# Performance work log

Measured on AMD Instinct MI355X. Metric: run time of the kernel, lower is better.

The kernel has to match this reference:

```python
import jax, jax.numpy as jnp
import numpy as np

B, S, E, H, STEPS = 32, 2048, 300, 256, 24


def setup_inputs() -> dict:
    key = jax.random.key(0)
    ks = jax.random.split(key, 16)
    sc = 0.05
    inp = {
        "input_ids": jax.random.normal(ks[0], (B, S, E), dtype=jnp.float32),
        "tree_ids": jax.random.randint(ks[1], (B, STEPS, S), 0, S),
        "tree_ids_r": jax.random.randint(ks[2], (B, STEPS, S), 0, S),
        "tree_ids_l": jax.random.randint(ks[3], (B, STEPS, S), 0, S),
        # N-ary (binary) TreeLSTM parameters (Tai et al. 2015)
        "W_iou": jax.random.normal(ks[4], (E, 3 * H), dtype=jnp.float32) * sc,
        "b_iou": jnp.zeros((3 * H,), dtype=jnp.float32),
        "U_iou_l": jax.random.normal(ks[5], (H, 3 * H), dtype=jnp.float32) * sc,
        "U_iou_r": jax.random.normal(ks[6], (H, 3 * H), dtype=jnp.float32) * sc,
        "W_f": jax.random.normal(ks[7], (E, H), dtype=jnp.float32) * sc,
        "b_f": jnp.zeros((H,), dtype=jnp.float32),
        "U_f_ll": jax.random.normal(ks[8], (H, H), dtype=jnp.float32) * sc,
        "U_f_lr": jax.random.normal(ks[9], (H, H), dtype=jnp.float32) * sc,
        "U_f_rl": jax.random.normal(ks[10], (H, H), dtype=jnp.float32) * sc,
        "U_f_rr": jax.random.normal(ks[11], (H, H), dtype=jnp.float32) * sc,
    }
    return inp


def _gather_nodes(t, idx):
    # t: [B,S,H], idx: [B,S] -> [B,S,H]
    return jnp.take_along_axis(t, idx[..., None], axis=1)


def reference(input_ids, tree_ids, tree_ids_r, tree_ids_l,
              W_iou, b_iou, U_iou_l, U_iou_r,
              W_f, b_f, U_f_ll, U_f_lr, U_f_rl, U_f_rr):
    dt = input_ids.dtype
    h0 = jnp.zeros((B, S, H), dtype=dt)
    c0 = jnp.zeros((B, S, H), dtype=dt)
    # input projections are step-invariant: compute once
    x_iou = input_ids @ W_iou + b_iou          # [B,S,3H]
    x_f = input_ids @ W_f + b_f                # [B,S,H]
    bidx = jnp.arange(B)[:, None]              # [B,1]

    def step(carry, ids):
        h, c = carry
        idd, idl, idr = ids                    # each [B,S]
        h_l = _gather_nodes(h, idl); c_l = _gather_nodes(c, idl)
        h_r = _gather_nodes(h, idr); c_r = _gather_nodes(c, idr)
        iou = x_iou + h_l @ U_iou_l + h_r @ U_iou_r
        i, o, u = jnp.split(iou, 3, axis=-1)
        i = jax.nn.sigmoid(i); o = jax.nn.sigmoid(o); u = jnp.tanh(u)
        f_l = jax.nn.sigmoid(x_f + h_l @ U_f_ll + h_r @ U_f_lr)
        f_r = jax.nn.sigmoid(x_f + h_l @ U_f_rl + h_r @ U_f_rr)
        c_new = i * u + f_l * c_l + f_r * c_r
        h_new = o * jnp.tanh(c_new)
        # scatter updates to destination node ids; slot 0 is the null slot
        h = h.at[bidx, idd].set(h_new)
        c = c.at[bidx, idd].set(c_new)
        h = h.at[:, 0].set(0.0)
        c = c.at[:, 0].set(0.0)
        return (h, c), None

    ids_seq = (jnp.transpose(tree_ids, (1, 0, 2)),
               jnp.transpose(tree_ids_l, (1, 0, 2)),
               jnp.transpose(tree_ids_r, (1, 0, 2)))
    (h, c), _ = jax.lax.scan(step, (h0, c0), ids_seq)

    roots = tree_ids[:, -1, :].max(axis=1)     # [B]
    h_root = jnp.take_along_axis(
        h, jnp.broadcast_to(roots[:, None, None], (B, 1, H)), axis=1)[:, 0]
    return (h, c, h_root)
```

## Files before the change

### kernel.cpp

```cpp
#include <hip/hip_runtime.h>
#include <hip/hip_bf16.h>
#include <math.h>

#define B_     32
#define S_     2048
#define E_     300
#define H_     256
#define STEPS_ 24
#define BS_    (B_ * S_)
#define NPACK  1280
#define KSL    16
#define KSLP   10
#define COPYB  1024

typedef __bf16 bf16x8 __attribute__((ext_vector_type(8)));
typedef float  f32x4  __attribute__((ext_vector_type(4)));

__device__ __forceinline__ float sigm(float x) {
    return 1.0f / (1.0f + __expf(-x));
}
__device__ __forceinline__ float fast_tanh(float x) {
    return 2.0f * sigm(2.0f * x) - 1.0f;
}

__global__ __launch_bounds__(256) void pack_B_kernel(
    const float* __restrict__ U_iou_l, const float* __restrict__ U_iou_r,
    const float* __restrict__ U_f_ll,  const float* __restrict__ U_f_lr,
    const float* __restrict__ U_f_rl,  const float* __restrict__ U_f_rr,
    __hip_bfloat16* __restrict__ Bp)
{
    const int idx = blockIdx.x * 256 + threadIdx.x;
    if (idx >= KSL * NPACK * 32) return;
    const int ks = idx / (NPACK * 32);
    const int rem = idx - ks * (NPACK * 32);
    const int p = rem >> 5;
    const int kin = rem & 31;
    const int k = ks * 32 + kin;
    const int w = p / 80;
    const int rg = p - w * 80;
    const int g = rg >> 4;
    const int c = w * 16 + (rg & 15);
    float v;
    if (g < 3) {
        const int col = g * 256 + c;
        v = (k < 256) ? U_iou_l[k * 768 + col] : U_iou_r[(k - 256) * 768 + col];
    } else if (g == 3) {
        v = (k < 256) ? U_f_ll[k * 256 + c] : U_f_lr[(k - 256) * 256 + c];
    } else {
        v = (k < 256) ? U_f_rl[k * 256 + c] : U_f_rr[(k - 256) * 256 + c];
    }
    Bp[idx] = __float2bfloat16(v);
}

__global__ __launch_bounds__(256) void pack_W_kernel(
    const float* __restrict__ W_iou, const float* __restrict__ W_f,
    __hip_bfloat16* __restrict__ Wp)
{
    const int idx = blockIdx.x * 256 + threadIdx.x;
    if (idx >= KSLP * 1024 * 32) return;
    const int ks = idx / (1024 * 32);
    const int rem = idx - ks * (1024 * 32);
    const int p = rem >> 5;
    const int kin = rem & 31;
    const int k = ks * 32 + kin;
    const int cw = p >> 6;
    const int g = (p >> 4) & 3;
    const int col = cw * 16 + (p & 15);
    float v = 0.f;
    if (k < E_) v = (g < 3) ? W_iou[k * 768 + g * 256 + col] : W_f[k * 256 + col];
    Wp[idx] = __float2bfloat16(v);
}

__global__ __launch_bounds__(256) void winner_kernel(
    const int* __restrict__ tree_ids, int* __restrict__ winner)
{
    const int idx = blockIdx.x * 256 + threadIdx.x;
    if (idx >= B_ * STEPS_ * S_) return;
    const int b = idx / (STEPS_ * S_);
    const int rem = idx - b * (STEPS_ * S_);
    const int t = rem / S_;
    const int s = rem - t * S_;
    const int d = tree_ids[idx];
    if ((unsigned)d < (unsigned)S_)
        atomicMax(&winner[(size_t)t * BS_ + b * S_ + d], s);
}

__global__ __launch_bounds__(256) void compact_kernel(
    const int* __restrict__ winner, int* __restrict__ compact,
    int* __restrict__ count)
{
    const int tb = blockIdx.x;
    const int tid = threadIdx.x;
    const int* w = winner + (size_t)tb * S_;
    int* cmp = compact + (size_t)tb * S_;
    __shared__ int scan_[256];
    __shared__ int base_;
    if (tid == 0) base_ = 0;
    __syncthreads();
    for (int chunk = 0; chunk < S_ / 256; ++chunk) {
        const int d = chunk * 256 + tid;
        const int s = w[d];
        const int p = (d != 0 && s >= 0) ? 1 : 0;
        int v = p;
        scan_[tid] = v;
        __syncthreads();
        for (int off = 1; off < 256; off <<= 1) {
            const int add = (tid >= off) ? scan_[tid - off] : 0;
            __syncthreads();
            v += add;
            scan_[tid] = v;
            __syncthreads();
        }
        const int mybase = base_;
        if (p) cmp[mybase + v - 1] = (s << 11) | d;
        __syncthreads();
        if (tid == 0) base_ += scan_[255];
        __syncthreads();
    }
    if (tid == 0) count[tb] = base_;
}

__global__ __launch_bounds__(256, 3) void proj_kernel(
    const float* __restrict__ input, const __hip_bfloat16* __restrict__ Wp,
    const float* __restrict__ b_iou, const float* __restrict__ b_f,
    __hip_bfloat16* __restrict__ x_pack)
{
    __shared__ __hip_bfloat16 Ash[64][328];
    const int tid = threadIdx.x;
    const int grp = blockIdx.x >> 5;
    const int l32 = blockIdx.x & 31;
    const int cb  = l32 >> 3;
    const int rg  = grp * 8 + (l32 & 7);
    const int row0 = rg * 64;

    for (int it = 0; it < 20; ++it) {
        const int idx = tid + it * 256;
        const int r = idx / 80;
        const int c4 = idx - r * 80;
        float4 v = make_float4(0.f, 0.f, 0.f, 0.f);
        if (c4 < 75) v = *(const float4*)(input + (size_t)(row0 + r) * E_ + c4 * 4);
        union { __hip_bfloat16 h[4]; uint2 u; } tconv;
        tconv.h[0] = __float2bfloat16(v.x);
        tconv.h[1] = __float2bfloat16(v.y);
        tconv.h[2] = __float2bfloat16(v.z);
        tconv.h[3] = __float2bfloat16(v.w);
        *(uint2*)&Ash[r][c4 * 4] = tconv.u;
    }
    __syncthreads();

    const int lane = tid & 63;
    const int wave = tid >> 6;
    const int m16 = lane & 15;
    const int q = lane >> 4;
    const int chunk = cb * 4 + wave;
    const int c = chunk * 16 + m16;

    f32x4 acc[4][4];
    const f32x4 z4 = {0.f, 0.f, 0.f, 0.f};
#pragma unroll
    for (int s = 0; s < 4; ++s)
#pragma unroll
        for (int g = 0; g < 4; ++g) acc[s][g] = z4;

    const __hip_bfloat16* wpb = Wp + ((size_t)(chunk * 64 + m16)) * 32 + q * 8;
    for (int ks = 0; ks < KSLP; ++ks) {
        bf16x8 bfrag[4];
#pragma unroll
        for (int g = 0; g < 4; ++g)
            bfrag[g] = *reinterpret_cast<const bf16x8*>(wpb + (size_t)ks * 32768 + g * 512);
        bf16x8 a[4];
#pragma unroll
        for (int s = 0; s < 4; ++s)
            a[s] = *reinterpret_cast<const bf16x8*>(&Ash[s * 16 + m16][ks * 32 + q * 8]);
#pragma unroll
        for (int s = 0; s < 4; ++s)
#pragma unroll
            for (int g = 0; g < 4; ++g)
                acc[s][g] = __builtin_amdgcn_mfma_f32_16x16x32_bf16(a[s], bfrag[g], acc[s][g], 0, 0, 0);
    }

    const float bi0 = b_iou[c];
    const float bi1 = b_iou[256 + c];
    const float bi2 = b_iou[512 + c];
    const float bf_ = b_f[c];
#pragma unroll
    for (int s = 0; s < 4; ++s) {
#pragma unroll
        for (int j = 0; j < 4; ++j) {
            const int row = row0 + s * 16 + q * 4 + j;
            const size_t xrow = (size_t)row * 1024;
            union { __hip_bfloat16 h[4]; uint2 u; } pk;
            pk.h[0] = __float2bfloat16(acc[s][0][j] + bi0);
            pk.h[1] = __float2bfloat16(acc[s][1][j] + bi1);
            pk.h[2] = __float2bfloat16(acc[s][2][j] + bi2);
            pk.h[3] = __float2bfloat16(acc[s][3][j] + bf_);
            *(uint2*)(x_pack + xrow + (size_t)c * 4) = pk.u;
        }
    }
}

__global__ __launch_bounds__(256, 4) void step_kernel(
    const __hip_bfloat16* __restrict__ h_cur, const __hip_bfloat16* __restrict__ c_cur,
    __hip_bfloat16* __restrict__ h_next, __hip_bfloat16* __restrict__ c_next,
    const int* __restrict__ tree_ids_l, const int* __restrict__ tree_ids_r,
    const int* __restrict__ winner_t, const int* __restrict__ compact,
    const int* __restrict__ count, const __hip_bfloat16* __restrict__ x_pack,
    const __hip_bfloat16* __restrict__ Bp, int t)
{
    const int tid = threadIdx.x;

    if (blockIdx.x < COPYB) {
        const uint4* h_cur4 = (const uint4*)h_cur;
        const uint4* c_cur4 = (const uint4*)c_cur;
        uint4* h_next4 = (uint4*)h_next;
        uint4* c_next4 = (uint4*)c_next;
#pragma unroll
        for (int i = 0; i < 8; ++i) {
            const int idx = blockIdx.x * 256 + tid + i * (COPYB * 256);
            const int row = idx >> 5;
            const int d = row & (S_ - 1);
            if (d == 0) {
                const uint4 z = make_uint4(0u, 0u, 0u, 0u);
                h_next4[idx] = z;
                c_next4[idx] = z;
            } else if (winner_t[row] < 0) {
                h_next4[idx] = h_cur4[idx];
                c_next4[idx] = c_cur4[idx];
            }
        }
        return;
    }

    const int sb     = blockIdx.x - COPYB;
    const int grp    = sb >> 5;
    const int l32    = sb & 31;
    const int nq     = l32 >> 3;
    const int tile_g = grp * 8 + (l32 & 7);
    const int b    = tile_g >> 6;
    const int tile = tile_g & 63;
    const int nAct = count[t * B_ + b];
    const int s0 = tile * 32;
    if (s0 >= nAct) return;

    __shared__ __hip_bfloat16 Ash[32][520];
    __shared__ int sS[32], sD[32], sIdl[32], sIdr[32];

    const int* cmp = compact + ((size_t)(t * B_ + b)) * S_;
    if (tid < 32) {
        const int gi = s0 + tid;
        const int pair = (gi < nAct) ? cmp[gi] : 0;
        sS[tid] = pair >> 11;
        sD[tid] = pair & 2047;
    }
    __syncthreads();

    const int* idl_b = tree_ids_l + ((size_t)b * STEPS_ + t) * S_;
    const int* idr_b = tree_ids_r + ((size_t)b * STEPS_ + t) * S_;
    if (tid < 32)       sIdl[tid]      = idl_b[sS[tid]];
    else if (tid < 64)  sIdr[tid - 32] = idr_b[sS[tid - 32]];
    __syncthreads();

#pragma unroll
    for (int it = 0; it < 8; ++it) {
        const int idx = tid + it * 256;
        const int r = idx >> 6;
        const int ch = idx & 63;
        const int half = ch >> 5;
        const int c16 = ch & 31;
        const int src = half ? sIdr[r] : sIdl[r];
        const uint4 v = *(const uint4*)(h_cur + ((size_t)(b * S_) + src) * H_ + c16 * 8);
        *(uint4*)&Ash[r][half * 256 + c16 * 8] = v;
    }
    __syncthreads();

    const int lane = tid & 63;
    const int wave = tid >> 6;
    const int m16 = lane & 15;
    const int q = lane >> 4;
    const int w16 = nq * 4 + wave;
    const int cg = w16 * 16 + m16;

    f32x4 acc[2][5];
#pragma unroll
    for (int sm = 0; sm < 2; ++sm) {
#pragma unroll
        for (int j = 0; j < 4; ++j) {
            const int r = sm * 16 + q * 4 + j;
            float xi = 0.f, xo = 0.f, xu = 0.f, xf = 0.f;
            if (sD[r] != 0) {
                const size_t xrow = ((size_t)(b * S_ + sS[r])) * 1024;
                union { uint2 u; __hip_bfloat16 x[4]; } xv;
                xv.u = *(const uint2*)(x_pack + xrow + (size_t)cg * 4);
                xi = __bfloat162float(xv.x[0]);
                xo = __bfloat162float(xv.x[1]);
                xu = __bfloat162float(xv.x[2]);
                xf = __bfloat162float(xv.x[3]);
            }
            acc[sm][0][j] = xi;
            acc[sm][1][j] = xo;
            acc[sm][2][j] = xu;
            acc[sm][3][j] = xf;
            acc[sm][4][j] = xf;
        }
    }

    const __hip_bfloat16* bp_base =
        Bp + ((size_t)(w16 * 80 + m16)) * 32 + q * 8;

    for (int ks = 0; ks < KSL; ++ks) {
        const bf16x8 a0 = *reinterpret_cast<const bf16x8*>(&Ash[m16][ks * 32 + q * 8]);
        const bf16x8 a1 = *reinterpret_cast<const bf16x8*>(&Ash[16 + m16][ks * 32 + q * 8]);
        const __hip_bfloat16* bk = bp_base + (size_t)ks * (NPACK * 32);
        bf16x8 bfrag[5];
#pragma unroll
        for (int g = 0; g < 5; ++g)
            bfrag[g] = *reinterpret_cast<const bf16x8*>(bk + g * 512);
#pragma unroll
        for (int g = 0; g < 5; ++g) {
            acc[0][g] = __builtin_amdgcn_mfma_f32_16x16x32_bf16(a0, bfrag[g], acc[0][g], 0, 0, 0);
            acc[1][g] = __builtin_amdgcn_mfma_f32_16x16x32_bf16(a1, bfrag[g], acc[1][g], 0, 0, 0);
        }
    }

    const __hip_bfloat16* cb = c_cur + (size_t)(b * S_) * H_ + cg;
#pragma unroll
    for (int sm = 0; sm < 2; ++sm) {
#pragma unroll
        for (int j = 0; j < 4; ++j) {
            const int r = sm * 16 + q * 4 + j;
            const int d = sD[r];
            if (d == 0) continue;
            const size_t orow = ((size_t)(b * S_ + d)) * H_;
            const float ig = sigm(acc[sm][0][j]);
            const float og = sigm(acc[sm][1][j]);
            const float ug = fast_tanh(acc[sm][2][j]);
            const float fl = sigm(acc[sm][3][j]);
            const float fr = sigm(acc[sm][4][j]);
            const float cl = __bfloat162float(cb[(size_t)sIdl[r] * H_]);
            const float cr = __bfloat162float(cb[(size_t)sIdr[r] * H_]);
            const float cn = ig * ug + fl * cl + fr * cr;
            const float hn = og * fast_tanh(cn);
            c_next[orow + cg] = __float2bfloat16(cn);
            h_next[orow + cg] = __float2bfloat16(hn);
        }
    }
}

__global__ __launch_bounds__(256) void convert_kernel(
    const __hip_bfloat16* __restrict__ h, const __hip_bfloat16* __restrict__ c,
    float* __restrict__ out_h, float* __restrict__ out_c)
{
    const size_t i = ((size_t)blockIdx.x * 256 + threadIdx.x) * 8;
#pragma unroll
    for (int j = 0; j < 8; ++j) {
        out_h[i + j] = __bfloat162float(h[i + j]);
        out_c[i + j] = __bfloat162float(c[i + j]);
    }
}

__global__ __launch_bounds__(256) void root_kernel(
    const int* __restrict__ tree_ids,
    const __hip_bfloat16* __restrict__ h, float* __restrict__ h_root)
{
    const int b = blockIdx.x;
    const int tid = threadIdx.x;
    const int* ids = tree_ids + ((size_t)b * STEPS_ + (STEPS_ - 1)) * S_;
    __shared__ int red[256];
    int m = 0;
    for (int s = tid; s < S_; s += 256) m = max(m, ids[s]);
    red[tid] = m;
    __syncthreads();
    for (int off = 128; off > 0; off >>= 1) {
        if (tid < off) red[tid] = max(red[tid], red[tid + off]);
        __syncthreads();
    }
    const int root = red[0];
    h_root[(size_t)b * H_ + tid] =
        __bfloat162float(h[((size_t)(b * S_) + root) * H_ + tid]);
}

extern "C" void kernel_launch(void* const* d_in, const int* in_sizes, int n_in,
                              void* d_out, int out_size, void* d_ws, size_t ws_size,
                              hipStream_t stream)
{
    const float* input_ids  = (const float*)d_in[0];
    const int*   tree_ids   = (const int*)d_in[1];
    const int*   tree_ids_r = (const int*)d_in[2];
    const int*   tree_ids_l = (const int*)d_in[3];
    const float* W_iou   = (const float*)d_in[4];
    const float* b_iou   = (const float*)d_in[5];
    const float* U_iou_l = (const float*)d_in[6];
    const float* U_iou_r = (const float*)d_in[7];
    const float* W_f     = (const float*)d_in[8];
    const float* b_f     = (const float*)d_in[9];
    const float* U_f_ll  = (const float*)d_in[10];
    const float* U_f_lr  = (const float*)d_in[11];
    const float* U_f_rl  = (const float*)d_in[12];
    const float* U_f_rr  = (const float*)d_in[13];

    float* out = (float*)d_out;
    float* out_h = out;
    float* out_c = out + (size_t)BS_ * H_;
    float* out_root = out + (size_t)2 * BS_ * H_;

    char* ws = (char*)d_ws;
    __hip_bfloat16* x_pack = (__hip_bfloat16*)(ws);
    __hip_bfloat16* hA     = (__hip_bfloat16*)(ws + 134217728ull);
    __hip_bfloat16* cA     = (__hip_bfloat16*)(ws + 167772160ull);
    int*            winner = (int*)(ws + 201326592ull);
    __hip_bfloat16* Bp     = (__hip_bfloat16*)(ws + 207618048ull);
    __hip_bfloat16* Wp     = (__hip_bfloat16*)(ws + 208928768ull);
    __hip_bfloat16* hB     = (__hip_bfloat16*)out_h;
    __hip_bfloat16* cB     = (__hip_bfloat16*)out_c;
    int* compact = (int*)((char*)out_h + 33554432ull);
    int* cnt     = compact + (size_t)STEPS_ * B_ * S_;

    hipMemsetAsync(hA, 0, (size_t)BS_ * H_ * sizeof(__hip_bfloat16), stream);
    hipMemsetAsync(cA, 0, (size_t)BS_ * H_ * sizeof(__hip_bfloat16), stream);
    hipMemsetAsync(winner, 0xFF, (size_t)STEPS_ * BS_ * sizeof(int), stream);

    pack_B_kernel<<<(KSL * NPACK * 32 + 255) / 256, 256, 0, stream>>>(
        U_iou_l, U_iou_r, U_f_ll, U_f_lr, U_f_rl, U_f_rr, Bp);
    pack_W_kernel<<<(KSLP * 1024 * 32 + 255) / 256, 256, 0, stream>>>(W_iou, W_f, Wp);
    winner_kernel<<<(B_ * STEPS_ * S_) / 256, 256, 0, stream>>>(tree_ids, winner);
    compact_kernel<<<STEPS_ * B_, 256, 0, stream>>>(winner, compact, cnt);
    proj_kernel<<<(BS_ / 64) * 4, 256, 0, stream>>>(input_ids, Wp, b_iou, b_f, x_pack);

    for (int t = 0; t < STEPS_; ++t) {
        const __hip_bfloat16* hc = (t & 1) ? hB : hA;
        const __hip_bfloat16* cc = (t & 1) ? cB : cA;
        __hip_bfloat16*       hn = (t & 1) ? hA : hB;
        __hip_bfloat16*       cn = (t & 1) ? cA : cB;
        const int* wt = winner + (size_t)t * BS_;

        step_kernel<<<COPYB + B_ * 64 * 4, 256, 0, stream>>>(
            hc, cc, hn, cn, tree_ids_l, tree_ids_r, wt,
            compact, cnt, x_pack, Bp, t);
    }

    convert_kernel<<<(BS_ * H_ / 8) / 256, 256, 0, stream>>>(hA, cA, out_h, out_c);
    root_kernel<<<B_, 256, 0, stream>>>(tree_ids, hA, out_root);
}
```

Before: 4.677 ms.

## Use direct global-to-LDS loads and issue x/c prefetches before the MFMA loop

The x_pack projection loads and the left/right child c loads are issued early into registers, before the gather barrier, so their latency overlaps the h gather and the MFMA loop. The h-row gather into shared memory now uses global_load_lds, which writes straight to LDS without staging in VGPRs. Accumulators start at zero and x is added in the epilogue. This raises register pressure, and the x loads are no longer skipped for null-destination rows, which adds some memory traffic.

```diff
diff --git a/kernel.cpp b/kernel.cpp
--- a/kernel.cpp
+++ b/kernel.cpp
@@ -21,6 +21,14 @@
 }
 __device__ __forceinline__ float fast_tanh(float x) {
     return 2.0f * sigm(2.0f * x) - 1.0f;
+}
+__device__ __forceinline__ float bf16bits2f(unsigned short u) {
+    return __uint_as_float(((unsigned)u) << 16);
+}
+__device__ __forceinline__ void gload_lds16(const void* g, void* l) {
+    __builtin_amdgcn_global_load_lds(
+        (const __attribute__((address_space(1))) void*)g,
+        (__attribute__((address_space(3))) void*)l, 16, 0, 0);
 }
 
 __global__ __launch_bounds__(256) void pack_B_kernel(
@@ -254,25 +262,6 @@
     }
     __syncthreads();
 
-    const int* idl_b = tree_ids_l + ((size_t)b * STEPS_ + t) * S_;
-    const int* idr_b = tree_ids_r + ((size_t)b * STEPS_ + t) * S_;
-    if (tid < 32)       sIdl[tid]      = idl_b[sS[tid]];
-    else if (tid < 64)  sIdr[tid - 32] = idr_b[sS[tid - 32]];
-    __syncthreads();
-
-#pragma unroll
-    for (int it = 0; it < 8; ++it) {
-        const int idx = tid + it * 256;
-        const int r = idx >> 6;
-        const int ch = idx & 63;
-        const int half = ch >> 5;
-        const int c16 = ch & 31;
-        const int src = half ? sIdr[r] : sIdl[r];
-        const uint4 v = *(const uint4*)(h_cur + ((size_t)(b * S_) + src) * H_ + c16 * 8);
-        *(uint4*)&Ash[r][half * 256 + c16 * 8] = v;
-    }
-    __syncthreads();
-
     const int lane = tid & 63;
     const int wave = tid >> 6;
     const int m16 = lane & 15;
@@ -280,29 +269,53 @@
     const int w16 = nq * 4 + wave;
     const int cg = w16 * 16 + m16;
 
-    f32x4 acc[2][5];
-#pragma unroll
-    for (int sm = 0; sm < 2; ++sm) {
+    uint2 xv[2][4];
+#pragma unroll
+    for (int sm = 0; sm < 2; ++sm)
 #pragma unroll
         for (int j = 0; j < 4; ++j) {
             const int r = sm * 16 + q * 4 + j;
-            float xi = 0.f, xo = 0.f, xu = 0.f, xf = 0.f;
-            if (sD[r] != 0) {
-                const size_t xrow = ((size_t)(b * S_ + sS[r])) * 1024;
-                union { uint2 u; __hip_bfloat16 x[4]; } xv;
-                xv.u = *(const uint2*)(x_pack + xrow + (size_t)cg * 4);
-                xi = __bfloat162float(xv.x[0]);
-                xo = __bfloat162float(xv.x[1]);
-                xu = __bfloat162float(xv.x[2]);
-                xf = __bfloat162float(xv.x[3]);
-            }
-            acc[sm][0][j] = xi;
-            acc[sm][1][j] = xo;
-            acc[sm][2][j] = xu;
-            acc[sm][3][j] = xf;
-            acc[sm][4][j] = xf;
-        }
-    }
+            xv[sm][j] = *(const uint2*)(x_pack
+                + ((size_t)(b * S_ + sS[r])) * 1024 + (size_t)cg * 4);
+        }
+
+    const int* idl_b = tree_ids_l + ((size_t)b * STEPS_ + t) * S_;
+    const int* idr_b = tree_ids_r + ((size_t)b * STEPS_ + t) * S_;
+    if (tid < 32)       sIdl[tid]      = idl_b[sS[tid]];
+    else if (tid < 64)  sIdr[tid - 32] = idr_b[sS[tid - 32]];
+    __syncthreads();
+
+    unsigned short clb[2][4], crb[2][4];
+    const __hip_bfloat16* cbase = c_cur + (size_t)(b * S_) * H_ + cg;
+#pragma unroll
+    for (int sm = 0; sm < 2; ++sm)
+#pragma unroll
+        for (int j = 0; j < 4; ++j) {
+            const int r = sm * 16 + q * 4 + j;
+            clb[sm][j] = *(const unsigned short*)(cbase + (size_t)sIdl[r] * H_);
+            crb[sm][j] = *(const unsigned short*)(cbase + (size_t)sIdr[r] * H_);
+        }
+
+    {
+        const int half = lane >> 5;
+        const int c16 = lane & 31;
+#pragma unroll
+        for (int it = 0; it < 8; ++it) {
+            const int r = wave + it * 4;
+            const int src = half ? sIdr[r] : sIdl[r];
+            const __hip_bfloat16* g =
+                h_cur + ((size_t)(b * S_) + src) * H_ + c16 * 8;
+            gload_lds16(g, &Ash[r][0]);
+        }
+    }
+    __syncthreads();
+
+    f32x4 acc[2][5];
+    const f32x4 z4 = {0.f, 0.f, 0.f, 0.f};
+#pragma unroll
+    for (int sm = 0; sm < 2; ++sm)
+#pragma unroll
+        for (int g = 0; g < 5; ++g) acc[sm][g] = z4;
 
     const __hip_bfloat16* bp_base =
         Bp + ((size_t)(w16 * 80 + m16)) * 32 + q * 8;
@@ -322,7 +335,6 @@
         }
     }
 
-    const __hip_bfloat16* cb = c_cur + (size_t)(b * S_) * H_ + cg;
 #pragma unroll
     for (int sm = 0; sm < 2; ++sm) {
 #pragma unroll
@@ -331,13 +343,19 @@
             const int d = sD[r];
             if (d == 0) continue;
             const size_t orow = ((size_t)(b * S_ + d)) * H_;
-            const float ig = sigm(acc[sm][0][j]);
-            const float og = sigm(acc[sm][1][j]);
-            const float ug = fast_tanh(acc[sm][2][j]);
-            const float fl = sigm(acc[sm][3][j]);
-            const float fr = sigm(acc[sm][4][j]);
-            const float cl = __bfloat162float(cb[(size_t)sIdl[r] * H_]);
-            const float cr = __bfloat162float(cb[(size_t)sIdr[r] * H_]);
+            union { uint2 u; unsigned short x[4]; } xu;
+            xu.u = xv[sm][j];
+            const float xi = bf16bits2f(xu.x[0]);
+            const float xo = bf16bits2f(xu.x[1]);
+            const float xuu = bf16bits2f(xu.x[2]);
+            const float xf = bf16bits2f(xu.x[3]);
+            const float ig = sigm(acc[sm][0][j] + xi);
+            const float og = sigm(acc[sm][1][j] + xo);
+            const float ug = fast_tanh(acc[sm][2][j] + xuu);
+            const float fl = sigm(acc[sm][3][j] + xf);
+            const float fr = sigm(acc[sm][4][j] + xf);
+            const float cl = bf16bits2f(clb[sm][j]);
+            const float cr = bf16bits2f(crb[sm][j]);
             const float cn = ig * ug + fl * cl + fr * cr;
             const float hn = og * fast_tanh(cn);
             c_next[orow + cg] = __float2bfloat16(cn);
```

Result: faster. 4.326 ms (-7.5%).
